# Optimization experiments

Hardware: AMD Instinct MI355X
Metric: run time of the kernel (lower is better)

Reference implementation:

```python
import jax, jax.numpy as jnp
import numpy as np

N_NODES = 50000
N_EDGES = 800000
IN_FEATS = 128
HIDDEN = 128
DNN_H = 256
N_CLASSES = 40


def setup_inputs() -> dict:
    key = jax.random.key(0)
    ks = jax.random.split(key, 12)
    features = jax.random.normal(ks[0], (N_NODES, IN_FEATS), dtype=jnp.float32)
    src = jax.random.randint(ks[1], (N_EDGES,), 0, N_NODES, dtype=jnp.int32)
    dst = jax.random.randint(ks[2], (N_EDGES,), 0, N_NODES, dtype=jnp.int32)
    def lin(k, fi, fo):
        s = 1.0 / np.sqrt(fi)
        return jax.random.uniform(k, (fi, fo), jnp.float32, -s, s)
    W1 = lin(ks[3], IN_FEATS, HIDDEN)
    b1 = jnp.zeros((HIDDEN,), jnp.float32)
    W2 = lin(ks[4], HIDDEN, HIDDEN)
    b2 = jnp.zeros((HIDDEN,), jnp.float32)
    Wd1 = lin(ks[5], HIDDEN, DNN_H)
    bd1 = jnp.zeros((DNN_H,), jnp.float32)
    Wd2 = lin(ks[6], DNN_H, N_CLASSES)
    bd2 = jnp.zeros((N_CLASSES,), jnp.float32)
    return {"features": features, "src": src, "dst": dst,
            "W1": W1, "b1": b1, "W2": W2, "b2": b2,
            "Wd1": Wd1, "bd1": bd1, "Wd2": Wd2, "bd2": bd2}


def _graph_conv(x, src, dst, W, b):
    # dgl GraphConv, norm='both': D_out^{-1/2} -> sum-aggregate -> D_in^{-1/2} -> linear -> relu
    ones = jnp.ones((src.shape[0],), x.dtype)
    deg_out = jax.ops.segment_sum(ones, src, num_segments=N_NODES)
    deg_in = jax.ops.segment_sum(ones, dst, num_segments=N_NODES)
    inv_sqrt_out = jax.lax.rsqrt(jnp.maximum(deg_out, 1.0))  # clamp zero-degree to 1 like dgl
    inv_sqrt_in = jax.lax.rsqrt(jnp.maximum(deg_in, 1.0))
    x = x * inv_sqrt_out[:, None]
    h = jax.ops.segment_sum(x[src], dst, num_segments=N_NODES)  # [N, d] sparse SpMM
    h = h * inv_sqrt_in[:, None]
    return jax.nn.relu(h @ W + b)


def reference(features, src, dst, W1, b1, W2, b2, Wd1, bd1, Wd2, bd2):
    h = _graph_conv(features, src, dst, W1, b1)   # dropout = identity (eval)
    h = _graph_conv(h, src, dst, W2, b2)
    # DNN: Linear -> LeakyReLU(0.01) -> (dropout identity), x2
    h = jax.nn.leaky_relu(h @ Wd1 + bd1, negative_slope=0.01)
    h = jax.nn.leaky_relu(h @ Wd2 + bd2, negative_slope=0.01)
    return h
```

## Files before the change

### kernel.cpp

```cpp
#include <hip/hip_runtime.h>


#define SCAN_B 256

typedef __attribute__((ext_vector_type(8))) short short8v;
typedef __attribute__((ext_vector_type(4))) float f32x4;

__global__ void k_scanA(const int* __restrict__ deg_in, int* __restrict__ incl,
                        int* __restrict__ bsum, int N) {
    __shared__ int s[SCAN_B];
    int t = threadIdx.x, i = blockIdx.x * SCAN_B + t;
    int v = (i < N) ? deg_in[i] : 0;
    s[t] = v; __syncthreads();
    for (int o = 1; o < SCAN_B; o <<= 1) {
        int x = (t >= o) ? s[t - o] : 0;
        __syncthreads();
        s[t] += x;
        __syncthreads();
    }
    if (i < N) incl[i] = s[t];
    if (t == SCAN_B - 1) bsum[blockIdx.x] = s[t];
}

__global__ void k_scanB(int* __restrict__ bsum, int NB) {
    __shared__ int s[SCAN_B];
    int t = threadIdx.x;
    int v = (t < NB) ? bsum[t] : 0;
    s[t] = v; __syncthreads();
    for (int o = 1; o < SCAN_B; o <<= 1) {
        int x = (t >= o) ? s[t - o] : 0;
        __syncthreads();
        s[t] += x;
        __syncthreads();
    }
    if (t < NB) bsum[t] = s[t] - v;
}

__global__ void k_scanC(const int* __restrict__ deg_in, const int* __restrict__ deg_out,
                        int* __restrict__ row_ptr, const int* __restrict__ bsum,
                        float* __restrict__ inv_in, float* __restrict__ inv_out,
                        int N, int E) {
    int t = threadIdx.x, i = blockIdx.x * SCAN_B + t;
    if (i < N) {
        int di = deg_in[i];
        row_ptr[i] = row_ptr[i] - di + bsum[blockIdx.x];
        inv_in[i]  = rsqrtf(fmaxf((float)di, 1.0f));
        inv_out[i] = rsqrtf(fmaxf((float)deg_out[i], 1.0f));
    }
    if (i == 0) row_ptr[N] = E;
}

__global__ void k_scatter3(const int* __restrict__ src, const int* __restrict__ dst,
                           const int* __restrict__ row_ptr, const int* __restrict__ rank,
                           const float* __restrict__ inv_out,
                           int2* __restrict__ edges, int E) {
    int i = blockIdx.x * blockDim.x + threadIdx.x;
    if (i < E) {
        int s = src[i];
        int2 p;
        p.x = s;
        p.y = __float_as_int(inv_out[s]);
        edges[row_ptr[dst[i]] + rank[i]] = p;
    }
}

__global__ void k_gather2(const float* __restrict__ X, const int2* __restrict__ edges,
                          const int* __restrict__ row_ptr, const float* __restrict__ inv_in,
                          const float* __restrict__ bias, float* __restrict__ Y, int N) {
    int lane = threadIdx.x & 31;
    int row = blockIdx.x * 8 + (threadIdx.x >> 5);
    if (row >= N) return;
    int rs = row_ptr[row], re = row_ptr[row + 1];
    float4 acc = {0.f, 0.f, 0.f, 0.f};
    int e = rs;
    #define LDROW(s) (*reinterpret_cast<const float4*>(&X[(size_t)(s) * 128 + lane * 4]))
    for (; e + 4 <= re; e += 4) {
        int2 p0 = edges[e], p1 = edges[e + 1], p2 = edges[e + 2], p3 = edges[e + 3];
        float4 x0 = LDROW(p0.x), x1 = LDROW(p1.x), x2 = LDROW(p2.x), x3 = LDROW(p3.x);
        float c0 = __int_as_float(p0.y), c1 = __int_as_float(p1.y);
        float c2 = __int_as_float(p2.y), c3 = __int_as_float(p3.y);
        acc.x += c0 * x0.x + c1 * x1.x + c2 * x2.x + c3 * x3.x;
        acc.y += c0 * x0.y + c1 * x1.y + c2 * x2.y + c3 * x3.y;
        acc.z += c0 * x0.z + c1 * x1.z + c2 * x2.z + c3 * x3.z;
        acc.w += c0 * x0.w + c1 * x1.w + c2 * x2.w + c3 * x3.w;
    }
    for (; e < re; ++e) {
        int2 p = edges[e];
        float c = __int_as_float(p.y);
        float4 xv = LDROW(p.x);
        acc.x += c * xv.x; acc.y += c * xv.y; acc.z += c * xv.z; acc.w += c * xv.w;
    }
    #undef LDROW
    float si = inv_in[row];
    float4 b4 = *reinterpret_cast<const float4*>(&bias[lane * 4]);
    float4 o;
    o.x = fmaxf(fmaf(acc.x, si, b4.x), 0.f);
    o.y = fmaxf(fmaf(acc.y, si, b4.y), 0.f);
    o.z = fmaxf(fmaf(acc.z, si, b4.z), 0.f);
    o.w = fmaxf(fmaf(acc.w, si, b4.w), 0.f);
    *reinterpret_cast<float4*>(&Y[(size_t)row * 128 + lane * 4]) = o;
}

__device__ inline unsigned short bf16_rne(float f) {
    unsigned int u = __float_as_uint(f);
    u += 0x7fffu + ((u >> 16) & 1u);
    return (unsigned short)(u >> 16);
}

__device__ inline void split1(float a, unsigned short& h, unsigned short& l) {
    unsigned short hh = bf16_rne(a);
    float hf = __uint_as_float((unsigned int)hh << 16);
    l = bf16_rne(a - hf);
    h = hh;
}

template<int K, int N, int ACT, bool DEG>
__global__ __launch_bounds__(256) void k_gemm_mfma(const float* __restrict__ A,
                                                   const float* __restrict__ W,
                                                   const float* __restrict__ bias,
                                                   float* __restrict__ C, int M,
                                                   const int* __restrict__ src,
                                                   const int* __restrict__ dst,
                                                   int* __restrict__ deg_out,
                                                   int* __restrict__ deg_in,
                                                   int* __restrict__ rank, int E, int epb,
                                                   int gmm, int degb) {
    __shared__ unsigned short Bh[64 * K], Bl[64 * K];
    __shared__ unsigned short Ah[128 * 32], Al[128 * 32];

    int t = threadIdx.x;
    int m0, cb;
    if (DEG) {
        int bid = blockIdx.x;
        if (bid < degb) {
            int base = bid * epb;
            int end = min(E, base + epb);
            for (int i = base + t; i < end; i += 256) {
                atomicAdd(&deg_out[src[i]], 1);
                rank[i] = atomicAdd(&deg_in[dst[i]], 1);
            }
            return;
        }
        int tile = bid - degb;
        m0 = (tile % gmm) * 128;
        cb = (tile / gmm) * 64;
    } else {
        m0 = blockIdx.x * 128;
        cb = blockIdx.y * 64;
    }

    {
        int c = t & 63;
        int kb = (t >> 6) * (K / 4);
        bool cok = (N % 64 == 0) || (cb + c < N);
        for (int j = 0; j < K / 4; ++j) {
            int k = kb + j;
            float v = cok ? W[(size_t)k * N + cb + c] : 0.f;
            unsigned short hi, lo; split1(v, hi, lo);
            int byte = (c * 2 * K + 2 * k) ^ ((c & 7) << 4);
            Bh[byte >> 1] = hi;
            Bl[byte >> 1] = lo;
        }
    }

    f32x4 acc[4][2];
    #pragma unroll
    for (int i = 0; i < 4; ++i)
        #pragma unroll
        for (int j = 0; j < 2; ++j)
            acc[i][j] = (f32x4){0.f, 0.f, 0.f, 0.f};

    int lane = t & 63;
    int wave = t >> 6;
    int wm = wave >> 1, wn = wave & 1;
    int lr = lane & 15, lg = lane >> 4;

    for (int kt = 0; kt < K / 32; ++kt) {
        __syncthreads();
        #pragma unroll
        for (int i = 0; i < 4; ++i) {
            int g = i * 256 + t;
            int r = g >> 3;
            int kq = (g & 7) * 4;
            int gr = m0 + r;
            float4 v = {0.f, 0.f, 0.f, 0.f};
            if (gr < M) v = *reinterpret_cast<const float4*>(&A[(size_t)gr * K + kt * 32 + kq]);
            ushort4 h4, l4;
            split1(v.x, h4.x, l4.x);
            split1(v.y, h4.y, l4.y);
            split1(v.z, h4.z, l4.z);
            split1(v.w, h4.w, l4.w);
            int byte = (r * 64 + 2 * kq) ^ ((r & 7) << 4);
            *reinterpret_cast<ushort4*>(&Ah[byte >> 1]) = h4;
            *reinterpret_cast<ushort4*>(&Al[byte >> 1]) = l4;
        }
        __syncthreads();

        short8v bhf[2], blf[2];
        #pragma unroll
        for (int nf = 0; nf < 2; ++nf) {
            int c = wn * 32 + nf * 16 + lr;
            int byte = (c * 2 * K + 2 * (kt * 32 + lg * 8)) ^ ((c & 7) << 4);
            bhf[nf] = *reinterpret_cast<const short8v*>(&Bh[byte >> 1]);
            blf[nf] = *reinterpret_cast<const short8v*>(&Bl[byte >> 1]);
        }
        #pragma unroll
        for (int mf = 0; mf < 4; ++mf) {
            int r = wm * 64 + mf * 16 + lr;
            int byte = (r * 64 + 2 * (lg * 8)) ^ ((r & 7) << 4);
            short8v ahf = *reinterpret_cast<const short8v*>(&Ah[byte >> 1]);
            short8v alf = *reinterpret_cast<const short8v*>(&Al[byte >> 1]);
            #pragma unroll
            for (int nf = 0; nf < 2; ++nf) {
                acc[mf][nf] = __builtin_amdgcn_mfma_f32_16x16x32_bf16(ahf, bhf[nf], acc[mf][nf], 0, 0, 0);
                acc[mf][nf] = __builtin_amdgcn_mfma_f32_16x16x32_bf16(ahf, blf[nf], acc[mf][nf], 0, 0, 0);
                acc[mf][nf] = __builtin_amdgcn_mfma_f32_16x16x32_bf16(alf, bhf[nf], acc[mf][nf], 0, 0, 0);
            }
        }
    }

    #pragma unroll
    for (int mf = 0; mf < 4; ++mf) {
        #pragma unroll
        for (int nf = 0; nf < 2; ++nf) {
            int col = cb + wn * 32 + nf * 16 + lr;
            if ((N % 64 != 0) && col >= N) continue;
            float bv = (ACT < 2) ? bias[col] : 0.f;
            #pragma unroll
            for (int rg = 0; rg < 4; ++rg) {
                int row = m0 + wm * 64 + mf * 16 + lg * 4 + rg;
                if (row < M) {
                    float v = acc[mf][nf][rg];
                    if (ACT == 0) v = fmaxf(v + bv, 0.f);
                    else if (ACT == 1) { v += bv; v = (v > 0.f) ? v : 0.01f * v; }
                    C[(size_t)row * N + col] = v;
                }
            }
        }
    }
}

extern "C" void kernel_launch(void* const* d_in, const int* in_sizes, int n_in,
                              void* d_out, int out_size, void* d_ws, size_t ws_size,
                              hipStream_t stream) {
    const float* feat = (const float*)d_in[0];
    const int*   src  = (const int*)d_in[1];
    const int*   dst  = (const int*)d_in[2];
    const float* W1   = (const float*)d_in[3];
    const float* b1   = (const float*)d_in[4];
    const float* W2   = (const float*)d_in[5];
    const float* b2   = (const float*)d_in[6];
    const float* Wd1  = (const float*)d_in[7];
    const float* bd1  = (const float*)d_in[8];
    const float* Wd2  = (const float*)d_in[9];
    const float* bd2  = (const float*)d_in[10];
    float* out = (float*)d_out;

    const int N = in_sizes[0] / 128;
    const int E = in_sizes[1];

    char* ws = (char*)d_ws;
    size_t off = 0;
    auto alloc = [&](size_t bytes) -> void* {
        void* p = ws + off;
        off += (bytes + 255) & ~(size_t)255;
        return p;
    };
    int* deg_out  = (int*)alloc((size_t)N * 4);
    int* deg_in   = (int*)alloc((size_t)N * 4);
    int* row_ptr  = (int*)alloc((size_t)(N + 1) * 4);
    int* bsum     = (int*)alloc(SCAN_B * 4);
    int* rank     = (int*)alloc((size_t)E * 4);
    int2* edges   = (int2*)alloc((size_t)E * 8);
    float* inv_out = (float*)alloc((size_t)N * 4);
    float* inv_in  = (float*)alloc((size_t)N * 4);
    float* bufA = (float*)alloc((size_t)N * 128 * 4);
    float* bufB = (float*)alloc((size_t)N * 128 * 4);
    float* hd   = (float*)alloc((size_t)N * 256 * 4);

    size_t zspan = (char*)deg_in + (size_t)N * 4 - (char*)deg_out;
    hipMemsetAsync(deg_out, 0, zspan, stream);

    int gE = (E + 255) / 256;
    int gN = (N + SCAN_B - 1) / SCAN_B;
    int gG = (N + 7) / 8;
    int gMM = (N + 127) / 128;

    const int DEGB = 512;
    int epb = (E + DEGB - 1) / DEGB;
    k_gemm_mfma<128, 128, 2, true><<<DEGB + gMM * 2, 256, 0, stream>>>(
        feat, W1, nullptr, bufA, N, src, dst, deg_out, deg_in, rank, E, epb, gMM, DEGB);

    k_scanA<<<gN, SCAN_B, 0, stream>>>(deg_in, row_ptr, bsum, N);
    k_scanB<<<1, SCAN_B, 0, stream>>>(bsum, gN);
    k_scanC<<<gN, SCAN_B, 0, stream>>>(deg_in, deg_out, row_ptr, bsum, inv_in, inv_out, N, E);
    k_scatter3<<<gE, 256, 0, stream>>>(src, dst, row_ptr, rank, inv_out, edges, E);

    k_gather2<<<gG, 256, 0, stream>>>(bufA, edges, row_ptr, inv_in, b1, bufB, N);
    k_gemm_mfma<128, 128, 2, false><<<dim3(gMM, 2), 256, 0, stream>>>(
        bufB, W2, nullptr, bufA, N, nullptr, nullptr, nullptr, nullptr, nullptr, 0, 0, 0, 0);
    k_gather2<<<gG, 256, 0, stream>>>(bufA, edges, row_ptr, inv_in, b2, bufB, N);
    k_gemm_mfma<128, 256, 1, false><<<dim3(gMM, 4), 256, 0, stream>>>(
        bufB, Wd1, bd1, hd, N, nullptr, nullptr, nullptr, nullptr, nullptr, 0, 0, 0, 0);
    k_gemm_mfma<256, 40, 1, false><<<dim3(gMM, 1), 256, 0, stream>>>(
        hd, Wd2, bd2, out, N, nullptr, nullptr, nullptr, nullptr, nullptr, 0, 0, 0, 0);
}
```

Before: 337.1 us.

## Replace atomic-rank CSR build with two-pass radix bucketing by destination

```diff
diff --git a/kernel.cpp b/kernel.cpp
--- a/kernel.cpp
+++ b/kernel.cpp
@@ -1,66 +1,99 @@
 #include <hip/hip_runtime.h>
 
-
-#define SCAN_B 256
 
 typedef __attribute__((ext_vector_type(8))) short short8v;
 typedef __attribute__((ext_vector_type(4))) float f32x4;
 
-__global__ void k_scanA(const int* __restrict__ deg_in, int* __restrict__ incl,
-                        int* __restrict__ bsum, int N) {
-    __shared__ int s[SCAN_B];
-    int t = threadIdx.x, i = blockIdx.x * SCAN_B + t;
-    int v = (i < N) ? deg_in[i] : 0;
-    s[t] = v; __syncthreads();
-    for (int o = 1; o < SCAN_B; o <<= 1) {
-        int x = (t >= o) ? s[t - o] : 0;
-        __syncthreads();
-        s[t] += x;
-        __syncthreads();
-    }
-    if (i < N) incl[i] = s[t];
-    if (t == SCAN_B - 1) bsum[blockIdx.x] = s[t];
-}
-
-__global__ void k_scanB(int* __restrict__ bsum, int NB) {
-    __shared__ int s[SCAN_B];
+__device__ inline unsigned short bf16_rne(float f) {
+    unsigned int u = __float_as_uint(f);
+    u += 0x7fffu + ((u >> 16) & 1u);
+    return (unsigned short)(u >> 16);
+}
+
+__device__ inline void split1(float a, unsigned short& h, unsigned short& l) {
+    unsigned short hh = bf16_rne(a);
+    float hf = __uint_as_float((unsigned int)hh << 16);
+    l = bf16_rne(a - hf);
+    h = hh;
+}
+
+__global__ void k_scanH(int* __restrict__ hist, int* __restrict__ bucket_base, int HB) {
+    __shared__ int tot[256], sc[256];
     int t = threadIdx.x;
-    int v = (t < NB) ? bsum[t] : 0;
-    s[t] = v; __syncthreads();
-    for (int o = 1; o < SCAN_B; o <<= 1) {
-        int x = (t >= o) ? s[t - o] : 0;
-        __syncthreads();
-        s[t] += x;
-        __syncthreads();
-    }
-    if (t < NB) bsum[t] = s[t] - v;
-}
-
-__global__ void k_scanC(const int* __restrict__ deg_in, const int* __restrict__ deg_out,
-                        int* __restrict__ row_ptr, const int* __restrict__ bsum,
-                        float* __restrict__ inv_in, float* __restrict__ inv_out,
-                        int N, int E) {
-    int t = threadIdx.x, i = blockIdx.x * SCAN_B + t;
-    if (i < N) {
-        int di = deg_in[i];
-        row_ptr[i] = row_ptr[i] - di + bsum[blockIdx.x];
-        inv_in[i]  = rsqrtf(fmaxf((float)di, 1.0f));
-        inv_out[i] = rsqrtf(fmaxf((float)deg_out[i], 1.0f));
-    }
-    if (i == 0) row_ptr[N] = E;
-}
-
-__global__ void k_scatter3(const int* __restrict__ src, const int* __restrict__ dst,
-                           const int* __restrict__ row_ptr, const int* __restrict__ rank,
-                           const float* __restrict__ inv_out,
-                           int2* __restrict__ edges, int E) {
+    int c = 0;
+    for (int blk = 0; blk < HB; ++blk) {
+        int v = hist[t * HB + blk];
+        hist[t * HB + blk] = c;
+        c += v;
+    }
+    tot[t] = c; sc[t] = c; __syncthreads();
+    for (int o = 1; o < 256; o <<= 1) {
+        int x = (t >= o) ? sc[t - o] : 0;
+        __syncthreads();
+        sc[t] += x;
+        __syncthreads();
+    }
+    bucket_base[t] = sc[t] - tot[t];
+    if (t == 255) bucket_base[256] = sc[255];
+}
+
+__global__ void k_invout(const int* __restrict__ deg_out, float* __restrict__ inv_out, int N) {
     int i = blockIdx.x * blockDim.x + threadIdx.x;
-    if (i < E) {
-        int s = src[i];
-        int2 p;
-        p.x = s;
-        p.y = __float_as_int(inv_out[s]);
-        edges[row_ptr[dst[i]] + rank[i]] = p;
+    if (i < N) inv_out[i] = rsqrtf(fmaxf((float)deg_out[i], 1.0f));
+}
+
+__global__ __launch_bounds__(256) void k_split(const int* __restrict__ src,
+                                               const int* __restrict__ dst,
+                                               const int* __restrict__ hist,
+                                               const int* __restrict__ bucket_base,
+                                               int2* __restrict__ tmp, int E, int HB, int hchunk) {
+    __shared__ int boff[256];
+    __shared__ int cnt[256];
+    int t = threadIdx.x, hb = blockIdx.x;
+    boff[t] = bucket_base[t] + hist[t * HB + hb];
+    cnt[t] = 0;
+    __syncthreads();
+    int base = hb * hchunk, end = min(E, base + hchunk);
+    for (int i = base + t; i < end; i += 256) {
+        int d = dst[i];
+        int bin = ((unsigned)d) >> 8;
+        int r = atomicAdd(&cnt[bin], 1);
+        tmp[boff[bin] + r] = make_int2(d, src[i]);
+    }
+}
+
+__global__ __launch_bounds__(256) void k_group(const int2* __restrict__ tmp,
+                                               const int* __restrict__ bucket_base,
+                                               const float* __restrict__ inv_out,
+                                               int2* __restrict__ edges, int* __restrict__ row_ptr,
+                                               float* __restrict__ inv_in, int N) {
+    __shared__ int bins[256], sc[256], cnt[256];
+    int t = threadIdx.x, b = blockIdx.x;
+    int lo = bucket_base[b], hi = bucket_base[b + 1];
+    bins[t] = 0; cnt[t] = 0;
+    __syncthreads();
+    for (int i = lo + t; i < hi; i += 256) atomicAdd(&bins[tmp[i].x & 255], 1);
+    __syncthreads();
+    sc[t] = bins[t]; __syncthreads();
+    for (int o = 1; o < 256; o <<= 1) {
+        int x = (t >= o) ? sc[t - o] : 0;
+        __syncthreads();
+        sc[t] += x;
+        __syncthreads();
+    }
+    int excl = sc[t] - bins[t];
+    int node = b * 256 + t;
+    if (node <= N) row_ptr[node] = lo + excl;
+    if (node < N) inv_in[node] = rsqrtf(fmaxf((float)bins[t], 1.0f));
+    __syncthreads();
+    sc[t] = excl;
+    __syncthreads();
+    for (int i = lo + t; i < hi; i += 256) {
+        int2 p = tmp[i];
+        int bin = p.x & 255;
+        int r = atomicAdd(&cnt[bin], 1);
+        int s = p.y;
+        edges[lo + sc[bin] + r] = make_int2(s, __float_as_int(inv_out[s]));
     }
 }
 
@@ -101,20 +134,7 @@
     *reinterpret_cast<float4*>(&Y[(size_t)row * 128 + lane * 4]) = o;
 }
 
-__device__ inline unsigned short bf16_rne(float f) {
-    unsigned int u = __float_as_uint(f);
-    u += 0x7fffu + ((u >> 16) & 1u);
-    return (unsigned short)(u >> 16);
-}
-
-__device__ inline void split1(float a, unsigned short& h, unsigned short& l) {
-    unsigned short hh = bf16_rne(a);
-    float hf = __uint_as_float((unsigned int)hh << 16);
-    l = bf16_rne(a - hf);
-    h = hh;
-}
-
-template<int K, int N, int ACT, bool DEG>
+template<int K, int N, int ACT, bool FRONT>
 __global__ __launch_bounds__(256) void k_gemm_mfma(const float* __restrict__ A,
                                                    const float* __restrict__ W,
                                                    const float* __restrict__ bias,
@@ -122,26 +142,36 @@
                                                    const int* __restrict__ src,
                                                    const int* __restrict__ dst,
                                                    int* __restrict__ deg_out,
-                                                   int* __restrict__ deg_in,
-                                                   int* __restrict__ rank, int E, int epb,
-                                                   int gmm, int degb) {
+                                                   int* __restrict__ hist,
+                                                   int E, int degb, int epb,
+                                                   int hb_n, int hchunk, int gmm) {
     __shared__ unsigned short Bh[64 * K], Bl[64 * K];
     __shared__ unsigned short Ah[128 * 32], Al[128 * 32];
 
     int t = threadIdx.x;
     int m0, cb;
-    if (DEG) {
+    if (FRONT) {
         int bid = blockIdx.x;
         if (bid < degb) {
             int base = bid * epb;
             int end = min(E, base + epb);
-            for (int i = base + t; i < end; i += 256) {
+            for (int i = base + t; i < end; i += 256)
                 atomicAdd(&deg_out[src[i]], 1);
-                rank[i] = atomicAdd(&deg_in[dst[i]], 1);
-            }
             return;
         }
-        int tile = bid - degb;
+        if (bid < degb + hb_n) {
+            int hb = bid - degb;
+            int* bins = (int*)Bh;
+            bins[t] = 0;
+            __syncthreads();
+            int base = hb * hchunk, end = min(E, base + hchunk);
+            for (int i = base + t; i < end; i += 256)
+                atomicAdd(&bins[((unsigned)dst[i]) >> 8], 1);
+            __syncthreads();
+            hist[t * hb_n + hb] = bins[t];
+            return;
+        }
+        int tile = bid - degb - hb_n;
         m0 = (tile % gmm) * 128;
         cb = (tile / gmm) * 64;
     } else {
@@ -259,6 +289,9 @@
     const int N = in_sizes[0] / 128;
     const int E = in_sizes[1];
 
+    const int DEGB = 512;
+    const int HB = 128;
+
     char* ws = (char*)d_ws;
     size_t off = 0;
     auto alloc = [&](size_t bytes) -> void* {
@@ -266,42 +299,40 @@
         off += (bytes + 255) & ~(size_t)255;
         return p;
     };
-    int* deg_out  = (int*)alloc((size_t)N * 4);
-    int* deg_in   = (int*)alloc((size_t)N * 4);
-    int* row_ptr  = (int*)alloc((size_t)(N + 1) * 4);
-    int* bsum     = (int*)alloc(SCAN_B * 4);
-    int* rank     = (int*)alloc((size_t)E * 4);
-    int2* edges   = (int2*)alloc((size_t)E * 8);
-    float* inv_out = (float*)alloc((size_t)N * 4);
-    float* inv_in  = (float*)alloc((size_t)N * 4);
+    int* deg_out     = (int*)alloc((size_t)N * 4);
+    int* hist        = (int*)alloc((size_t)256 * HB * 4);
+    int* bucket_base = (int*)alloc(257 * 4);
+    int* row_ptr     = (int*)alloc((size_t)(N + 1) * 4);
+    int2* edges      = (int2*)alloc((size_t)E * 8);
+    float* inv_out   = (float*)alloc((size_t)N * 4);
+    float* inv_in    = (float*)alloc((size_t)N * 4);
     float* bufA = (float*)alloc((size_t)N * 128 * 4);
     float* bufB = (float*)alloc((size_t)N * 128 * 4);
     float* hd   = (float*)alloc((size_t)N * 256 * 4);
-
-    size_t zspan = (char*)deg_in + (size_t)N * 4 - (char*)deg_out;
-    hipMemsetAsync(deg_out, 0, zspan, stream);
-
-    int gE = (E + 255) / 256;
-    int gN = (N + SCAN_B - 1) / SCAN_B;
+    int2* tmp = (int2*)hd;
+
+    hipMemsetAsync(deg_out, 0, (size_t)N * 4, stream);
+
     int gG = (N + 7) / 8;
     int gMM = (N + 127) / 128;
-
-    const int DEGB = 512;
     int epb = (E + DEGB - 1) / DEGB;
-    k_gemm_mfma<128, 128, 2, true><<<DEGB + gMM * 2, 256, 0, stream>>>(
-        feat, W1, nullptr, bufA, N, src, dst, deg_out, deg_in, rank, E, epb, gMM, DEGB);
-
-    k_scanA<<<gN, SCAN_B, 0, stream>>>(deg_in, row_ptr, bsum, N);
-    k_scanB<<<1, SCAN_B, 0, stream>>>(bsum, gN);
-    k_scanC<<<gN, SCAN_B, 0, stream>>>(deg_in, deg_out, row_ptr, bsum, inv_in, inv_out, N, E);
-    k_scatter3<<<gE, 256, 0, stream>>>(src, dst, row_ptr, rank, inv_out, edges, E);
+    int hchunk = (E + HB - 1) / HB;
+    int gNB = (N + 255) / 256;
+
+    k_gemm_mfma<128, 128, 2, true><<<DEGB + HB + gMM * 2, 256, 0, stream>>>(
+        feat, W1, nullptr, bufA, N, src, dst, deg_out, hist, E, DEGB, epb, HB, hchunk, gMM);
+
+    k_scanH<<<1, 256, 0, stream>>>(hist, bucket_base, HB);
+    k_invout<<<(N + 255) / 256, 256, 0, stream>>>(deg_out, inv_out, N);
+    k_split<<<HB, 256, 0, stream>>>(src, dst, hist, bucket_base, tmp, E, HB, hchunk);
+    k_group<<<gNB, 256, 0, stream>>>(tmp, bucket_base, inv_out, edges, row_ptr, inv_in, N);
 
     k_gather2<<<gG, 256, 0, stream>>>(bufA, edges, row_ptr, inv_in, b1, bufB, N);
     k_gemm_mfma<128, 128, 2, false><<<dim3(gMM, 2), 256, 0, stream>>>(
-        bufB, W2, nullptr, bufA, N, nullptr, nullptr, nullptr, nullptr, nullptr, 0, 0, 0, 0);
+        bufB, W2, nullptr, bufA, N, nullptr, nullptr, nullptr, nullptr, 0, 0, 0, 0, 0, 0);
     k_gather2<<<gG, 256, 0, stream>>>(bufA, edges, row_ptr, inv_in, b2, bufB, N);
     k_gemm_mfma<128, 256, 1, false><<<dim3(gMM, 4), 256, 0, stream>>>(
-        bufB, Wd1, bd1, hd, N, nullptr, nullptr, nullptr, nullptr, nullptr, 0, 0, 0, 0);
+        bufB, Wd1, bd1, hd, N, nullptr, nullptr, nullptr, nullptr, 0, 0, 0, 0, 0, 0);
     k_gemm_mfma<256, 40, 1, false><<<dim3(gMM, 1), 256, 0, stream>>>(
-        hd, Wd2, bd2, out, N, nullptr, nullptr, nullptr, nullptr, nullptr, 0, 0, 0, 0);
-}
+        hd, Wd2, bd2, out, N, nullptr, nullptr, nullptr, nullptr, 0, 0, 0, 0, 0, 0);
+}
```

Result: slower. 368.3 us (+9.2%).
